# Kernel tuning notes

Measured on AMD Instinct MI355X. Metric: run time of the kernel, lower is better.

The kernel has to match this reference:

```python
import jax, jax.numpy as jnp
import numpy as np

B, T, H, E = 8, 2048, 512, 512

def setup_inputs() -> dict:
    key = jax.random.key(0)
    k1, k2, k3, k4 = jax.random.split(key, 4)
    tokens = jax.random.normal(k1, (B, T, H), dtype=jnp.float32)
    # Linear(hidden,embed,bias=False): stored as (in,out) so Q = tokens @ Wq
    Wq = jax.random.normal(k2, (H, E), dtype=jnp.float32) / np.sqrt(H)
    Wk = jax.random.normal(k3, (H, E), dtype=jnp.float32) / np.sqrt(H)
    Wv = jax.random.normal(k4, (H, H), dtype=jnp.float32) / np.sqrt(H)
    return {"tokens": tokens, "Wq": Wq, "Wk": Wk, "Wv": Wv}

def reference(tokens, Wq, Wk, Wv):
    Q = jnp.einsum('bth,he->bte', tokens, Wq)   # [B,T,E]
    K = jnp.einsum('bsh,he->bse', tokens, Wk)   # [B,T,E]
    V = jnp.einsum('bsh,hd->bsd', tokens, Wv)   # [B,T,H]
    scoremats = jnp.einsum('bte,bse->bts', Q, K)  # [B,T,T]
    # NOTE: softmax over axis=1 (query axis t), matching F.softmax(dim=1)
    attnmats = jax.nn.softmax(scoremats, axis=1)
    ctx_vecs = jnp.einsum('bts,bsh->bth', attnmats, V)  # [B,T,H]
    return ctx_vecs
```

## Files before the change

kernel.cpp:

```cpp
#include <hip/hip_runtime.h>

typedef _Float16 f16;
typedef _Float16 f16x8 __attribute__((ext_vector_type(8)));
typedef _Float16 f16x4 __attribute__((ext_vector_type(4)));
typedef float   f32x4 __attribute__((ext_vector_type(4)));

#define LOG2E 1.44269504088896340736f

__device__ __forceinline__ f32x4 mfma_f16(f16x8 a, f16x8 b, f32x4 c){
  return __builtin_amdgcn_mfma_f32_16x16x32_f16(a, b, c, 0, 0, 0);
}
__device__ __forceinline__ float fexp2(float x){ return __builtin_amdgcn_exp2f(x); }

__device__ __forceinline__ void gld16(void* lds, const void* g){
  __builtin_amdgcn_global_load_lds(
      (const __attribute__((address_space(1))) unsigned int*)g,
      (__attribute__((address_space(3))) unsigned int*)lds,
      16, 0, 0);
}

__global__ __launch_bounds__(256) void k_prep_g(const float* __restrict__ Wq,
                                                const float* __restrict__ Wk,
                                                f16* __restrict__ B16){
  __shared__ float ak[32][36];
  __shared__ float aq[32][36];
  const int n0 = blockIdx.y * 32, e0 = blockIdx.x * 32;
  const int u = threadIdx.x;
  const int ty = u >> 4, tx = u & 15;
  float acc[2][2] = {};
  for (int x0 = 0; x0 < 512; x0 += 32){
    __syncthreads();
    {
      int r = u >> 3, c4 = (u & 7) * 4;
      *(float4*)&ak[r][c4] = *(const float4*)&Wk[(n0 + r) * 512 + x0 + c4];
      *(float4*)&aq[r][c4] = *(const float4*)&Wq[(e0 + r) * 512 + x0 + c4];
    }
    __syncthreads();
#pragma unroll 8
    for (int x = 0; x < 32; ++x){
      float k0 = ak[ty * 2 + 0][x], k1 = ak[ty * 2 + 1][x];
      float q0 = aq[tx * 2 + 0][x], q1 = aq[tx * 2 + 1][x];
      acc[0][0] += k0 * q0; acc[0][1] += k0 * q1;
      acc[1][0] += k1 * q0; acc[1][1] += k1 * q1;
    }
  }
#pragma unroll
  for (int i = 0; i < 2; ++i)
#pragma unroll
    for (int j = 0; j < 2; ++j)
      B16[(size_t)(n0 + ty * 2 + i) * 512 + e0 + tx * 2 + j] = (f16)acc[i][j];
}

__global__ __launch_bounds__(256) void k_prep_wv(const float* __restrict__ Wv,
                                                 f16* __restrict__ B16){
  __shared__ float t[64][72];
  const int e0 = blockIdx.x * 64, h0 = blockIdx.y * 64;
  const int u = threadIdx.x;
#pragma unroll
  for (int k = 0; k < 4; ++k){
    int idx = u + k * 256; int r = idx >> 4, c4 = (idx & 15) * 4;
    *(float4*)&t[r][c4] = *(const float4*)&Wv[(e0 + r) * 512 + h0 + c4];
  }
  __syncthreads();
#pragma unroll
  for (int k = 0; k < 4; ++k){
    int idx = u + k * 256; int j = idx >> 4, i4 = (idx & 15) * 4;
#pragma unroll
    for (int c = 0; c < 4; ++c)
      B16[(size_t)(512 + h0 + j) * 512 + e0 + i4 + c] = (f16)t[i4 + c][j];
  }
}

__global__ __launch_bounds__(256) void k_cast(const float* __restrict__ tok,
                                              f16* __restrict__ T16){
  int i = blockIdx.x * 256 + threadIdx.x;
  const float4* p = (const float4*)tok + (size_t)i * 2;
  float4 a = p[0], b = p[1];
  f16x8 h;
  h[0] = (f16)a.x; h[1] = (f16)a.y; h[2] = (f16)a.z; h[3] = (f16)a.w;
  h[4] = (f16)b.x; h[5] = (f16)b.y; h[6] = (f16)b.z; h[7] = (f16)b.w;
  *((f16x8*)T16 + i) = h;
}

__global__ __launch_bounds__(256, 4) void k_gemm(const f16* __restrict__ T16,
                                                 const f16* __restrict__ B16,
                                                 f16* __restrict__ QG,
                                                 f16* __restrict__ VT){
  __shared__ __align__(16) f16 Abuf[2][128 * 32];
  __shared__ __align__(16) f16 Bbuf[2][128 * 32];
  const int tb = blockIdx.x, nb = blockIdx.y;
  const int u = threadIdx.x;
  const int w = u >> 6, l = u & 63, lr = l & 15, lq = l >> 4;
  const int l2 = l & 3, hi4 = l >> 2;
  const int wm = (w & 1) * 64, wn = (w >> 1) * 64;
  f32x4 acc[4][4] = {};
  auto stage = [&](int c, int buf){
    const f16* sa = T16 + (size_t)tb * 128 * 512 + c * 32;
    const f16* sb = B16 + (size_t)nb * 128 * 512 + c * 32;
#pragma unroll
    for (int k = 0; k < 2; ++k){
      int i = w * 2 + k;
      int row = i * 16 + hi4;
      gld16((char*)&Abuf[buf][0] + i * 1024, sa + (size_t)row * 512 + ((l2 ^ (row & 3)) * 8));
      gld16((char*)&Bbuf[buf][0] + i * 1024, sb + (size_t)row * 512 + ((l2 ^ (row & 3)) * 8));
    }
  };
  stage(0, 0);
  for (int c = 0; c < 16; ++c){
    __syncthreads();
    if (c < 15) stage(c + 1, (c + 1) & 1);
    const f16* A = &Abuf[c & 1][0];
    const f16* B = &Bbuf[c & 1][0];
    f16x8 af[4], bf[4];
#pragma unroll
    for (int mt = 0; mt < 4; ++mt){
      int row = wm + mt * 16 + lr;
      af[mt] = *(const f16x8*)((const char*)A + row * 64 + ((lq ^ (row & 3)) << 4));
    }
#pragma unroll
    for (int nt = 0; nt < 4; ++nt){
      int row = wn + nt * 16 + lr;
      bf[nt] = *(const f16x8*)((const char*)B + row * 64 + ((lq ^ (row & 3)) << 4));
    }
#pragma unroll
    for (int mt = 0; mt < 4; ++mt)
#pragma unroll
      for (int nt = 0; nt < 4; ++nt)
        acc[mt][nt] = mfma_f16(af[mt], bf[nt], acc[mt][nt]);
  }
  if (nb < 4){
#pragma unroll
    for (int mt = 0; mt < 4; ++mt)
#pragma unroll
      for (int nt = 0; nt < 4; ++nt){
        int n = nb * 128 + wn + nt * 16 + lr;
        int r0 = tb * 128 + wm + mt * 16 + lq * 4;
#pragma unroll
        for (int j = 0; j < 4; ++j)
          QG[(size_t)(r0 + j) * 512 + n] = (f16)acc[mt][nt][j];
      }
  } else {
#pragma unroll
    for (int mt = 0; mt < 4; ++mt)
#pragma unroll
      for (int nt = 0; nt < 4; ++nt){
        int h = (nb - 4) * 128 + wn + nt * 16 + lr;
        int r0 = tb * 128 + wm + mt * 16 + lq * 4;
        int bq = r0 >> 11, s = r0 & 2047;
        f16x4 hv;
#pragma unroll
        for (int j = 0; j < 4; ++j) hv[j] = (f16)acc[mt][nt][j];
        *(f16x4*)&VT[(size_t)(bq * 512 + h) * 2048 + s] = hv;
      }
  }
}

__global__ __launch_bounds__(256, 4) void k_pass1p(const f16* __restrict__ T16,
                                                   const f16* __restrict__ QG,
                                                   f16* __restrict__ Pp,
                                                   float* __restrict__ Mp,
                                                   float* __restrict__ Dp){
  const int gid = blockIdx.x;
  const int b = gid & 7;
  const int sb = (gid >> 3) & 15;
  const int tb = gid >> 7;
  const int u = threadIdx.x;
  const int w = u >> 6, l = u & 63, lr = l & 15, lq = l >> 4;
  const int l2 = l & 3, hi4 = l >> 2;
  const int wm = (w & 1) * 64, wn = (w >> 1) * 64;

  __shared__ __align__(16) f16 Abuf[2][128 * 32];
  __shared__ __align__(16) f16 Bbuf[2][128 * 32];
  __shared__ float redM[2][128];
  __shared__ float redD[2][128];

  f32x4 acc[4][4] = {};
  auto stage = [&](int c, int buf){
    const f16* sa = T16 + ((size_t)(b * 2048 + sb * 128) * 512 + c * 32);
    const f16* sb_ = QG + ((size_t)(b * 2048 + tb * 128) * 512 + c * 32);
#pragma unroll
    for (int k = 0; k < 2; ++k){
      int i = w * 2 + k;
      int row = i * 16 + hi4;
      gld16((char*)&Abuf[buf][0] + i * 1024, sa  + (size_t)row * 512 + ((l2 ^ (row & 3)) * 8));
      gld16((char*)&Bbuf[buf][0] + i * 1024, sb_ + (size_t)row * 512 + ((l2 ^ (row & 3)) * 8));
    }
  };
  stage(0, 0);
  for (int c = 0; c < 16; ++c){
    __syncthreads();
    if (c < 15) stage(c + 1, (c + 1) & 1);
    const f16* A = &Abuf[c & 1][0];
    const f16* B = &Bbuf[c & 1][0];
    f16x8 af[4], bf[4];
#pragma unroll
    for (int mt = 0; mt < 4; ++mt){
      int row = wm + mt * 16 + lr;
      af[mt] = *(const f16x8*)((const char*)A + row * 64 + ((lq ^ (row & 3)) << 4));
    }
#pragma unroll
    for (int nt = 0; nt < 4; ++nt){
      int row = wn + nt * 16 + lr;
      bf[nt] = *(const f16x8*)((const char*)B + row * 64 + ((lq ^ (row & 3)) << 4));
    }
#pragma unroll
    for (int mt = 0; mt < 4; ++mt)
#pragma unroll
      for (int nt = 0; nt < 4; ++nt)
        acc[mt][nt] = mfma_f16(af[mt], bf[nt], acc[mt][nt]);
  }
#pragma unroll
  for (int mt = 0; mt < 4; ++mt)
#pragma unroll
    for (int nt = 0; nt < 4; ++nt)
#pragma unroll
      for (int j = 0; j < 4; ++j)
        acc[mt][nt][j] *= LOG2E;
#pragma unroll
  for (int mt = 0; mt < 4; ++mt)
#pragma unroll
    for (int j = 0; j < 4; ++j){
      float m2 = fmaxf(fmaxf(acc[mt][0][j], acc[mt][1][j]),
                       fmaxf(acc[mt][2][j], acc[mt][3][j]));
#pragma unroll
      for (int off = 1; off <= 8; off <<= 1)
        m2 = fmaxf(m2, __shfl_xor(m2, off, 64));
      if (lr == 0) redM[w >> 1][wm + mt * 16 + lq * 4 + j] = m2;
    }
  __syncthreads();
  float M[4][4];
#pragma unroll
  for (int mt = 0; mt < 4; ++mt)
#pragma unroll
    for (int j = 0; j < 4; ++j){
      int idx = wm + mt * 16 + lq * 4 + j;
      M[mt][j] = fmaxf(redM[0][idx], redM[1][idx]);
    }
#pragma unroll
  for (int mt = 0; mt < 4; ++mt)
#pragma unroll
    for (int nt = 0; nt < 4; ++nt){
      int t = tb * 128 + wn + nt * 16 + lr;
      f16x4 h4;
#pragma unroll
      for (int j = 0; j < 4; ++j){
        float p = fexp2(acc[mt][nt][j] - M[mt][j]);
        acc[mt][nt][j] = p;
        h4[j] = (f16)p;
      }
      *(f16x4*)&Pp[(size_t)(b * 2048 + t) * 2048 + sb * 128 + wm + mt * 16 + lq * 4] = h4;
    }
#pragma unroll
  for (int mt = 0; mt < 4; ++mt)
#pragma unroll
    for (int j = 0; j < 4; ++j){
      float sd = acc[mt][0][j] + acc[mt][1][j] + acc[mt][2][j] + acc[mt][3][j];
#pragma unroll
      for (int off = 1; off <= 8; off <<= 1)
        sd += __shfl_xor(sd, off, 64);
      if (lr == 0) redD[w >> 1][wm + mt * 16 + lq * 4 + j] = sd;
    }
  __syncthreads();
  if (u < 128){
    int sg = b * 2048 + sb * 128 + u;
    Mp[tb * 16384 + sg] = fmaxf(redM[0][u], redM[1][u]);
    Dp[tb * 16384 + sg] = redD[0][u] + redD[1][u];
  }
}

__global__ __launch_bounds__(256) void k_scm(const float* __restrict__ Mp,
                                             const float* __restrict__ Dp,
                                             float* __restrict__ SC){
  int i = blockIdx.x * 256 + threadIdx.x;
  float mv[16];
  float m = -1e30f;
#pragma unroll
  for (int ti = 0; ti < 16; ++ti){
    mv[ti] = Mp[ti * 16384 + i];
    m = fmaxf(m, mv[ti]);
  }
  float d = 0.f;
#pragma unroll
  for (int ti = 0; ti < 16; ++ti)
    d += Dp[ti * 16384 + i] * fexp2(mv[ti] - m);
  float rd = 1.0f / d;
#pragma unroll
  for (int ti = 0; ti < 16; ++ti)
    SC[ti * 16384 + i] = fexp2(mv[ti] - m) * rd;
}

__global__ __launch_bounds__(256, 2) void k_pass2p(const f16* __restrict__ Pp,
                                                   const f16* __restrict__ VT,
                                                   const float* __restrict__ SC,
                                                   float* __restrict__ out){
  const int gid = blockIdx.x;
  const int b = gid & 7;
  const int tt = (gid >> 3) & 31;
  const int hh = gid >> 8;
  const int t0 = tt * 64;
  const int ti = tt >> 1;
  const int u = threadIdx.x;
  const int w = u >> 6, l = u & 63, lr = l & 15, lq = l >> 4;

  __shared__ __align__(16) f16 Pl[64 * 256];
  __shared__ __align__(16) f16 Vt[2][256 * 32];
  __shared__ float scl[256];

  f32x4 acc[4][4] = {};

  auto stagePl = [&](int si){
#pragma unroll
    for (int k = 0; k < 8; ++k){
      int i = w * 8 + k;
      int row = i * 2 + (l >> 5);
      int slot = l & 31;
      gld16((char*)Pl + i * 1024,
            Pp + ((size_t)(b * 2048 + t0 + row) * 2048 + si * 256 + ((slot ^ (row & 7)) * 8)));
    }
  };
  auto stageV = [&](int si, int sc_, int buf){
#pragma unroll
    for (int k = 0; k < 4; ++k){
      int i = w * 4 + k;
      int row = i * 16 + (l >> 2);
      gld16((char*)&Vt[buf][0] + i * 1024,
            VT + ((size_t)(b * 512 + hh * 256 + row) * 2048 + si * 256 + sc_ * 32 + (((l & 3) ^ (row & 3)) * 8)));
    }
  };

  for (int si = 0; si < 8; ++si){
    __syncthreads();
    stagePl(si);
    if (w == 0) gld16(scl, SC + ti * 16384 + b * 2048 + si * 256 + l * 4);
    __syncthreads();
    {
      int row = u >> 2;
#pragma unroll
      for (int k = 0; k < 8; ++k){
        int slot = (u & 3) * 8 + k;
        f16* p = (f16*)((char*)Pl + row * 512 + ((slot ^ (row & 7)) << 4));
        f16x8 v = *(f16x8*)p;
#pragma unroll
        for (int e = 0; e < 8; ++e)
          v[e] = (f16)((float)v[e] * scl[slot * 8 + e]);
        *(f16x8*)p = v;
      }
    }
    stageV(si, 0, 0);
    __syncthreads();
#pragma unroll
    for (int sc_ = 0; sc_ < 8; ++sc_){
      if (sc_ < 7) stageV(si, sc_ + 1, (sc_ + 1) & 1);
      const f16* V = &Vt[sc_ & 1][0];
      f16x8 vf[4], pf[4];
#pragma unroll
      for (int ht = 0; ht < 4; ++ht){
        int row = w * 64 + ht * 16 + lr;
        vf[ht] = *(const f16x8*)((const char*)V + row * 64 + ((lq ^ (row & 3)) << 4));
      }
#pragma unroll
      for (int nt = 0; nt < 4; ++nt){
        int row = nt * 16 + lr;
        pf[nt] = *(const f16x8*)((const char*)Pl + row * 512 + (((sc_ * 4 + lq) ^ (row & 7)) << 4));
      }
      __builtin_amdgcn_s_setprio(1);
#pragma unroll
      for (int ht = 0; ht < 4; ++ht)
#pragma unroll
        for (int nt = 0; nt < 4; ++nt)
          acc[ht][nt] = mfma_f16(vf[ht], pf[nt], acc[ht][nt]);
      __builtin_amdgcn_s_setprio(0);
      __syncthreads();
    }
  }
#pragma unroll
  for (int ht = 0; ht < 4; ++ht)
#pragma unroll
    for (int nt = 0; nt < 4; ++nt){
      int t = t0 + nt * 16 + lr;
      int h = hh * 256 + w * 64 + ht * 16 + lq * 4;
      float4 v;
      v.x = acc[ht][nt][0]; v.y = acc[ht][nt][1];
      v.z = acc[ht][nt][2]; v.w = acc[ht][nt][3];
      *(float4*)&out[(size_t)(b * 2048 + t) * 512 + h] = v;
    }
}

extern "C" void kernel_launch(void* const* d_in, const int* in_sizes, int n_in,
                              void* d_out, int out_size, void* d_ws, size_t ws_size,
                              hipStream_t stream){
  (void)in_sizes; (void)n_in; (void)out_size; (void)ws_size;
  const float* tokens = (const float*)d_in[0];
  const float* Wq = (const float*)d_in[1];
  const float* Wk = (const float*)d_in[2];
  const float* Wv = (const float*)d_in[3];
  char* ws = (char*)d_ws;
  f16*    T16 = (f16*)(ws);
  f16*    QG  = (f16*)(ws + (16u << 20));
  f16*    VT  = (f16*)(ws + (32u << 20));
  f16*    B16 = (f16*)(ws + (48u << 20));
  float*  SC  = (float*)(ws + (50u << 20));
  float*  Mp  = (float*)(ws + (51u << 20));
  float*  Dp  = (float*)(ws + (52u << 20));
  f16*    Pp  = (f16*)(ws + (54u << 20));
  float* out = (float*)d_out;

  k_prep_g <<<dim3(16, 16), dim3(256), 0, stream>>>(Wq, Wk, B16);
  k_prep_wv<<<dim3(8, 8),   dim3(256), 0, stream>>>(Wv, B16);
  k_cast   <<<dim3(4096),   dim3(256), 0, stream>>>(tokens, T16);
  k_gemm   <<<dim3(128, 8), dim3(256), 0, stream>>>(T16, B16, QG, VT);
  k_pass1p <<<dim3(2048),   dim3(256), 0, stream>>>(T16, QG, Pp, Mp, Dp);
  k_scm    <<<dim3(64),     dim3(256), 0, stream>>>(Mp, Dp, SC);
  k_pass2p <<<dim3(512),    dim3(256), 0, stream>>>(Pp, VT, SC, out);
}
```

Before: 196.3 us.

## Restructure pass2 as 128x128 tiled GEMM with on-the-fly fp16 softmax scaling

The second-pass kernel is rewritten as a 128(h) x 128(t) tile GEMM over 64 chunks of 32 along s, with double-buffered A/B staging. The column-softmax scale is now applied in registers to each P fragment as it is loaded, instead of rescaling the whole P tile in LDS between barriers. The scale factors are stored as fp16 and the whole per-block row of 2048 scales is loaded once, which cuts the extra LDS pass and halves the scale traffic. The occupancy hint rises to 4 blocks per CU. Risks are the small 32-wide k-chunk with a barrier on every step, and some precision loss from multiplying the scales in fp16.

```diff
diff --git a/kernel.cpp b/kernel.cpp
--- a/kernel.cpp
+++ b/kernel.cpp
@@ -270,7 +270,7 @@
 
 __global__ __launch_bounds__(256) void k_scm(const float* __restrict__ Mp,
                                              const float* __restrict__ Dp,
-                                             float* __restrict__ SC){
+                                             f16* __restrict__ SC16){
   int i = blockIdx.x * 256 + threadIdx.x;
   float mv[16];
   float m = -1e30f;
@@ -286,102 +286,76 @@
   float rd = 1.0f / d;
 #pragma unroll
   for (int ti = 0; ti < 16; ++ti)
-    SC[ti * 16384 + i] = fexp2(mv[ti] - m) * rd;
-}
-
-__global__ __launch_bounds__(256, 2) void k_pass2p(const f16* __restrict__ Pp,
+    SC16[ti * 16384 + i] = (f16)(fexp2(mv[ti] - m) * rd);
+}
+
+__global__ __launch_bounds__(256, 4) void k_pass2p(const f16* __restrict__ Pp,
                                                    const f16* __restrict__ VT,
-                                                   const float* __restrict__ SC,
+                                                   const f16* __restrict__ SC16,
                                                    float* __restrict__ out){
   const int gid = blockIdx.x;
   const int b = gid & 7;
-  const int tt = (gid >> 3) & 31;
-  const int hh = gid >> 8;
-  const int t0 = tt * 64;
-  const int ti = tt >> 1;
+  const int tb = (gid >> 3) & 15;
+  const int hb = gid >> 7;
   const int u = threadIdx.x;
   const int w = u >> 6, l = u & 63, lr = l & 15, lq = l >> 4;
-
-  __shared__ __align__(16) f16 Pl[64 * 256];
-  __shared__ __align__(16) f16 Vt[2][256 * 32];
-  __shared__ float scl[256];
-
+  const int l2 = l & 3, hi4 = l >> 2;
+  const int wm = (w & 1) * 64, wn = (w >> 1) * 64;
+
+  __shared__ __align__(16) f16 Abuf[2][128 * 32];
+  __shared__ __align__(16) f16 Bbuf[2][128 * 32];
+  __shared__ __align__(16) f16 scl[2048];
+
+  {
+    f16x8 v = *(const f16x8*)&SC16[(size_t)tb * 16384 + b * 2048 + u * 8];
+    *(f16x8*)&scl[u * 8] = v;
+  }
   f32x4 acc[4][4] = {};
-
-  auto stagePl = [&](int si){
-#pragma unroll
-    for (int k = 0; k < 8; ++k){
-      int i = w * 8 + k;
-      int row = i * 2 + (l >> 5);
-      int slot = l & 31;
-      gld16((char*)Pl + i * 1024,
-            Pp + ((size_t)(b * 2048 + t0 + row) * 2048 + si * 256 + ((slot ^ (row & 7)) * 8)));
+  auto stage = [&](int c, int buf){
+    const f16* sa = VT + ((size_t)(b * 512 + hb * 128) * 2048 + c * 32);
+    const f16* sb_ = Pp + ((size_t)(b * 2048 + tb * 128) * 2048 + c * 32);
+#pragma unroll
+    for (int k = 0; k < 2; ++k){
+      int i = w * 2 + k;
+      int row = i * 16 + hi4;
+      gld16((char*)&Abuf[buf][0] + i * 1024, sa  + (size_t)row * 2048 + ((l2 ^ (row & 3)) * 8));
+      gld16((char*)&Bbuf[buf][0] + i * 1024, sb_ + (size_t)row * 2048 + ((l2 ^ (row & 3)) * 8));
     }
   };
-  auto stageV = [&](int si, int sc_, int buf){
-#pragma unroll
-    for (int k = 0; k < 4; ++k){
-      int i = w * 4 + k;
-      int row = i * 16 + (l >> 2);
-      gld16((char*)&Vt[buf][0] + i * 1024,
-            VT + ((size_t)(b * 512 + hh * 256 + row) * 2048 + si * 256 + sc_ * 32 + (((l & 3) ^ (row & 3)) * 8)));
-    }
-  };
-
-  for (int si = 0; si < 8; ++si){
-    __syncthreads();
-    stagePl(si);
-    if (w == 0) gld16(scl, SC + ti * 16384 + b * 2048 + si * 256 + l * 4);
-    __syncthreads();
-    {
-      int row = u >> 2;
-#pragma unroll
-      for (int k = 0; k < 8; ++k){
-        int slot = (u & 3) * 8 + k;
-        f16* p = (f16*)((char*)Pl + row * 512 + ((slot ^ (row & 7)) << 4));
-        f16x8 v = *(f16x8*)p;
-#pragma unroll
-        for (int e = 0; e < 8; ++e)
-          v[e] = (f16)((float)v[e] * scl[slot * 8 + e]);
-        *(f16x8*)p = v;
-      }
-    }
-    stageV(si, 0, 0);
-    __syncthreads();
-#pragma unroll
-    for (int sc_ = 0; sc_ < 8; ++sc_){
-      if (sc_ < 7) stageV(si, sc_ + 1, (sc_ + 1) & 1);
-      const f16* V = &Vt[sc_ & 1][0];
-      f16x8 vf[4], pf[4];
-#pragma unroll
-      for (int ht = 0; ht < 4; ++ht){
-        int row = w * 64 + ht * 16 + lr;
-        vf[ht] = *(const f16x8*)((const char*)V + row * 64 + ((lq ^ (row & 3)) << 4));
-      }
-#pragma unroll
-      for (int nt = 0; nt < 4; ++nt){
-        int row = nt * 16 + lr;
-        pf[nt] = *(const f16x8*)((const char*)Pl + row * 512 + (((sc_ * 4 + lq) ^ (row & 7)) << 4));
-      }
-      __builtin_amdgcn_s_setprio(1);
-#pragma unroll
-      for (int ht = 0; ht < 4; ++ht)
-#pragma unroll
-        for (int nt = 0; nt < 4; ++nt)
-          acc[ht][nt] = mfma_f16(vf[ht], pf[nt], acc[ht][nt]);
-      __builtin_amdgcn_s_setprio(0);
-      __syncthreads();
-    }
-  }
-#pragma unroll
-  for (int ht = 0; ht < 4; ++ht)
-#pragma unroll
-    for (int nt = 0; nt < 4; ++nt){
-      int t = t0 + nt * 16 + lr;
-      int h = hh * 256 + w * 64 + ht * 16 + lq * 4;
+  stage(0, 0);
+  for (int c = 0; c < 64; ++c){
+    __syncthreads();
+    if (c < 63) stage(c + 1, (c + 1) & 1);
+    const f16* A = &Abuf[c & 1][0];
+    const f16* B = &Bbuf[c & 1][0];
+    f16x8 sclv = *(const f16x8*)&scl[c * 32 + lq * 8];
+    f16x8 af[4], bf[4];
+#pragma unroll
+    for (int mt = 0; mt < 4; ++mt){
+      int row = wm + mt * 16 + lr;
+      af[mt] = *(const f16x8*)((const char*)A + row * 64 + ((lq ^ (row & 3)) << 4));
+    }
+#pragma unroll
+    for (int nt = 0; nt < 4; ++nt){
+      int row = wn + nt * 16 + lr;
+      f16x8 p = *(const f16x8*)((const char*)B + row * 64 + ((lq ^ (row & 3)) << 4));
+      bf[nt] = p * sclv;
+    }
+#pragma unroll
+    for (int mt = 0; mt < 4; ++mt)
+#pragma unroll
+      for (int nt = 0; nt < 4; ++nt)
+        acc[mt][nt] = mfma_f16(af[mt], bf[nt], acc[mt][nt]);
+  }
+#pragma unroll
+  for (int mt = 0; mt < 4; ++mt)
+#pragma unroll
+    for (int nt = 0; nt < 4; ++nt){
+      int t = tb * 128 + wn + nt * 16 + lr;
+      int h = hb * 128 + wm + mt * 16 + lq * 4;
       float4 v;
-      v.x = acc[ht][nt][0]; v.y = acc[ht][nt][1];
-      v.z = acc[ht][nt][2]; v.w = acc[ht][nt][3];
+      v.x = acc[mt][nt][0]; v.y = acc[mt][nt][1];
+      v.z = acc[mt][nt][2]; v.w = acc[mt][nt][3];
       *(float4*)&out[(size_t)(b * 2048 + t) * 512 + h] = v;
     }
 }
@@ -399,7 +373,7 @@
   f16*    QG  = (f16*)(ws + (16u << 20));
   f16*    VT  = (f16*)(ws + (32u << 20));
   f16*    B16 = (f16*)(ws + (48u << 20));
-  float*  SC  = (float*)(ws + (50u << 20));
+  f16*    SC16= (f16*)(ws + (50u << 20));
   float*  Mp  = (float*)(ws + (51u << 20));
   float*  Dp  = (float*)(ws + (52u << 20));
   f16*    Pp  = (f16*)(ws + (54u << 20));
@@ -410,6 +384,6 @@
   k_cast   <<<dim3(4096),   dim3(256), 0, stream>>>(tokens, T16);
   k_gemm   <<<dim3(128, 8), dim3(256), 0, stream>>>(T16, B16, QG, VT);
   k_pass1p <<<dim3(2048),   dim3(256), 0, stream>>>(T16, QG, Pp, Mp, Dp);
-  k_scm    <<<dim3(64),     dim3(256), 0, stream>>>(Mp, Dp, SC);
-  k_pass2p <<<dim3(512),    dim3(256), 0, stream>>>(Pp, VT, SC, out);
-}
+  k_scm    <<<dim3(64),     dim3(256), 0, stream>>>(Mp, Dp, SC16);
+  k_pass2p <<<dim3(512),    dim3(256), 0, stream>>>(Pp, VT, SC16, out);
+}
```

After: 178.7 us. 1.1x faster.
